# Performance work log

Hardware: AMD Instinct MI355X
Metric: run time of the kernel (lower is better)

Reference implementation:

```python
import jax, jax.numpy as jnp
import numpy as np

NUM_HEADS = 12
ALPHA = 0.5
TANH_CLIP = 5.0


def setup_inputs() -> dict:
    key = jax.random.key(0)
    k1, k2, k3, k4, k5 = jax.random.split(key, 5)
    B, N, C = 8, 1024, 768
    x = jax.random.normal(k1, (B, N, C), dtype=jnp.float32)
    # qkv: Linear(C -> 3C), proj: Linear(C -> C); torch stores weight as [out, in]
    s = 1.0 / np.sqrt(C)
    qkv_w = jax.random.normal(k2, (3 * C, C), dtype=jnp.float32) * s
    qkv_b = jax.random.normal(k3, (3 * C,), dtype=jnp.float32) * 0.02
    proj_w = jax.random.normal(k4, (C, C), dtype=jnp.float32) * s
    proj_b = jax.random.normal(k5, (C,), dtype=jnp.float32) * 0.02
    return {"x": x, "qkv_w": qkv_w, "qkv_b": qkv_b, "proj_w": proj_w, "proj_b": proj_b}


def reference(x, qkv_w, qkv_b, proj_w, proj_b):
    B, N, C = x.shape
    H = NUM_HEADS
    D = C // H
    scale = D ** -0.5
    # qkv projection -> [B, N, 3, H, D] -> q/k/v each [B, H, N, D]
    qkv = (x @ qkv_w.T + qkv_b).reshape(B, N, 3, H, D)
    qkv = jnp.transpose(qkv, (2, 0, 3, 1, 4))
    q, k, v = qkv[0], qkv[1], qkv[2]
    # pre-softmax scores [B, H, N, N]
    scores = jnp.einsum("bhnd,bhmd->bhnm", q * scale, k)
    scores_t = jnp.swapaxes(scores, -2, -1)
    scores_sym = 0.5 * (scores + scores_t)
    scores_asym = 0.5 * (scores - scores_t)
    scores = scores_sym + ALPHA * scores_asym
    # gamma_mode == 'approx'
    gamma = np.sqrt((1.0 + ALPHA ** 2) / 2.0)
    scores = scores / gamma
    # tanh clip
    scores = TANH_CLIP * jnp.tanh(scores / TANH_CLIP)
    attn = jax.nn.softmax(scores, axis=-1)
    out = jnp.einsum("bhnm,bhmd->bhnd", attn, v)  # [B, H, N, D]
    out = jnp.transpose(out, (0, 2, 1, 3)).reshape(B, N, C)
    return out @ proj_w.T + proj_b
```

## Files before the change

### kernel.cpp

```cpp
#include <hip/hip_runtime.h>
#include <hip/hip_bf16.h>
#include <stdint.h>

typedef unsigned short u16;
typedef __attribute__((ext_vector_type(8))) short bf16x8;
typedef __attribute__((ext_vector_type(4))) float f32x4;

#define LDS_AS(p) ((__attribute__((address_space(3))) void*)(p))
#define GLB_AS(p) ((__attribute__((address_space(1))) void*)(p))

__device__ __forceinline__ u16 f2bf(float f) {
  union { float f; uint32_t u; } v; v.f = f;
  uint32_t u = v.u;
  u += 0x7fffu + ((u >> 16) & 1u);
  return (u16)(u >> 16);
}

__device__ __forceinline__ float exp2_fast(float x) {
  float r;
  asm("v_exp_f32 %0, %1" : "=v"(r) : "v"(x));
  return r;
}

__device__ __forceinline__ float bits2f(uint32_t u) {
  union { uint32_t u; float f; } v; v.u = u; return v.f;
}
__device__ __forceinline__ uint32_t f2bits(float f) {
  union { float f; uint32_t u; } v; v.f = f; return v.u;
}
__device__ __forceinline__ uint32_t pack_hi16(uint32_t lo_src, uint32_t hi_src) {
  return __builtin_amdgcn_perm(hi_src, lo_src, 0x07060302u);
}

__device__ __forceinline__ void cvt8(const float* __restrict__ s, u16* __restrict__ d) {
  const float4* sv = (const float4*)s;
  float4 a = sv[0], b = sv[1];
  uint4 o;
  o.x = (uint32_t)f2bf(a.x) | ((uint32_t)f2bf(a.y) << 16);
  o.y = (uint32_t)f2bf(a.z) | ((uint32_t)f2bf(a.w) << 16);
  o.z = (uint32_t)f2bf(b.x) | ((uint32_t)f2bf(b.y) << 16);
  o.w = (uint32_t)f2bf(b.z) | ((uint32_t)f2bf(b.w) << 16);
  *(uint4*)d = o;
}

__global__ __launch_bounds__(256) void k_convert(
    const float* __restrict__ x, const float* __restrict__ wq, const float* __restrict__ wp,
    u16* __restrict__ xb, u16* __restrict__ wqb, u16* __restrict__ wpb) {
  int tid = blockIdx.x * 256 + threadIdx.x;
  int np  = gridDim.x * 256;
  for (int i = tid; i < (8192*768)/8; i += np) cvt8(x  + (size_t)i*8, xb  + (size_t)i*8);
  for (int i = tid; i < (2304*768)/8; i += np) cvt8(wq + (size_t)i*8, wqb + (size_t)i*8);
  for (int i = tid; i < (768*768)/8;  i += np) cvt8(wp + (size_t)i*8, wpb + (size_t)i*8);
}

template<bool SWAP>
__device__ __forceinline__ void gemm_core(const u16* __restrict__ A,
                                          const u16* __restrict__ B,
                                          u16* As, u16* Bs,
                                          int rowA0, int rowB0,
                                          f32x4 acc[4][4]) {
  const int t  = threadIdx.x;
  const int lane = t & 63;
  const int wv = t >> 6;
  const int wr = wv >> 1, wc = wv & 1;
  const int lr = lane & 15, lg = lane >> 4;

#define GSTAGE(KT, BUF)                                                                         \
  {                                                                                             \
    _Pragma("unroll")                                                                           \
    for (int p = 0; p < 2; ++p) {                                                               \
      int idx = p * 256 + t;                                                                    \
      int row = idx >> 2;                                                                       \
      int cc  = (idx & 3) ^ ((row >> 1) & 3);                                                   \
      __builtin_amdgcn_global_load_lds(GLB_AS(A + (size_t)(rowA0 + row) * 768 + (KT) * 32 + cc * 8), \
                                       LDS_AS(As + (BUF) * 4096 + idx * 8), 16, 0, 0);          \
    }                                                                                           \
    _Pragma("unroll")                                                                           \
    for (int p = 0; p < 2; ++p) {                                                               \
      int idx = p * 256 + t;                                                                    \
      int row = idx >> 2;                                                                       \
      int cc  = (idx & 3) ^ ((row >> 1) & 3);                                                   \
      __builtin_amdgcn_global_load_lds(GLB_AS(B + (size_t)(rowB0 + row) * 768 + (KT) * 32 + cc * 8), \
                                       LDS_AS(Bs + (BUF) * 4096 + idx * 8), 16, 0, 0);          \
    }                                                                                           \
  }

  GSTAGE(0, 0);

#pragma unroll 1
  for (int kt = 0; kt < 24; ++kt) {
    const int cur = kt & 1;
    __syncthreads();

    if (kt < 23) GSTAGE(kt + 1, cur ^ 1);

    const u16* Ab = As + cur * 4096;
    const u16* Bb = Bs + cur * 4096;
    bf16x8 af[4], bf_[4];
#pragma unroll
    for (int mi = 0; mi < 4; ++mi) {
      int row = wr * 64 + mi * 16 + lr;
      int cc  = lg ^ ((row >> 1) & 3);
      af[mi] = *(const bf16x8*)(Ab + row * 32 + cc * 8);
    }
#pragma unroll
    for (int ni = 0; ni < 4; ++ni) {
      int row = wc * 64 + ni * 16 + lr;
      int cc  = lg ^ ((row >> 1) & 3);
      bf_[ni] = *(const bf16x8*)(Bb + row * 32 + cc * 8);
    }
#pragma unroll
    for (int mi = 0; mi < 4; ++mi)
#pragma unroll
      for (int ni = 0; ni < 4; ++ni) {
        if (SWAP)
          acc[mi][ni] = __builtin_amdgcn_mfma_f32_16x16x32_bf16(bf_[ni], af[mi], acc[mi][ni], 0, 0, 0);
        else
          acc[mi][ni] = __builtin_amdgcn_mfma_f32_16x16x32_bf16(af[mi], bf_[ni], acc[mi][ni], 0, 0, 0);
      }
  }
#undef GSTAGE
}

__global__ __launch_bounds__(256) void k_gemm_qkv(
    const u16* __restrict__ Aq, const u16* __restrict__ Bw, const float* __restrict__ bias,
    u16* __restrict__ Qh, u16* __restrict__ Kh, u16* __restrict__ Vt) {
  __shared__ u16 As[2 * 128 * 32];
  __shared__ u16 Bs[2 * 128 * 32];
  int bid = blockIdx.x;
  int wg  = (bid & 7) * 144 + (bid >> 3);
  int bx  = wg % 18, by = wg / 18;

  const int t = threadIdx.x, lane = t & 63, wv = t >> 6;
  const int wr = wv >> 1, wc = wv & 1, lr = lane & 15, lg = lane >> 4;
  const int tsec = bx / 6;
  const int colBase = bx * 128 + wc * 64;

  const float gam = 0.7905694150420949f;
  const float rC1 = __builtin_sqrtf(0.57707801636f);
  const float sc1 = __builtin_sqrtf(0.09375f / gam) * rC1;
  const float sc2 = __builtin_sqrtf(0.03125f / gam) * rC1;

  f32x4 acc[4][4];
#pragma unroll
  for (int mi = 0; mi < 4; ++mi)
#pragma unroll
    for (int ni = 0; ni < 4; ++ni) acc[mi][ni] = (f32x4){0.f, 0.f, 0.f, 0.f};

  if (tsec < 2) {
    gemm_core<true>(Aq, Bw, As, Bs, by * 128, bx * 128, acc);

    float4 bv4[4];
#pragma unroll
    for (int ni = 0; ni < 4; ++ni)
      bv4[ni] = *(const float4*)(bias + colBase + ni * 16 + lg * 4);

#pragma unroll
    for (int mi = 0; mi < 4; ++mi) {
      int n = by * 128 + wr * 64 + mi * 16 + lr;
      int b = n >> 10, nn = n & 1023;
#pragma unroll
      for (int ni = 0; ni < 4; ++ni) {
        int fs = colBase - tsec * 768 + ni * 16 + lg * 4;
        int h = fs >> 6, d = fs & 63;
        size_t rowq = ((size_t)(b * 12 + h) * 1024 + nn) * 128;
        float v0 = acc[mi][ni][0] + bv4[ni].x;
        float v1 = acc[mi][ni][1] + bv4[ni].y;
        float v2 = acc[mi][ni][2] + bv4[ni].z;
        float v3 = acc[mi][ni][3] + bv4[ni].w;
        uint2 wq_, wk_;
        wq_.x = (uint32_t)f2bf(v0 * sc1) | ((uint32_t)f2bf(v1 * sc1) << 16);
        wq_.y = (uint32_t)f2bf(v2 * sc1) | ((uint32_t)f2bf(v3 * sc1) << 16);
        wk_.x = (uint32_t)f2bf(v0 * sc2) | ((uint32_t)f2bf(v1 * sc2) << 16);
        wk_.y = (uint32_t)f2bf(v2 * sc2) | ((uint32_t)f2bf(v3 * sc2) << 16);
        if (tsec == 0) {
          *(uint2*)(Qh + rowq + d)      = wq_;
          *(uint2*)(Kh + rowq + 64 + d) = wk_;
        } else {
          *(uint2*)(Kh + rowq + d)      = wq_;
          *(uint2*)(Qh + rowq + 64 + d) = wk_;
        }
      }
    }
  } else {
    gemm_core<false>(Aq, Bw, As, Bs, by * 128, bx * 128, acc);

    float bv[4];
#pragma unroll
    for (int ni = 0; ni < 4; ++ni) bv[ni] = bias[colBase + ni * 16 + lr];

#pragma unroll
    for (int mi = 0; mi < 4; ++mi) {
      int tok0 = by * 128 + wr * 64 + mi * 16 + lg * 4;
      int b = tok0 >> 10, n0 = tok0 & 1023;
#pragma unroll
      for (int ni = 0; ni < 4; ++ni) {
        int fs = colBase - 2 * 768 + ni * 16 + lr;
        int h = fs >> 6, d = fs & 63;
        float v0 = acc[mi][ni][0] + bv[ni];
        float v1 = acc[mi][ni][1] + bv[ni];
        float v2 = acc[mi][ni][2] + bv[ni];
        float v3 = acc[mi][ni][3] + bv[ni];
        uint2 w;
        w.x = (uint32_t)f2bf(v0) | ((uint32_t)f2bf(v1) << 16);
        w.y = (uint32_t)f2bf(v2) | ((uint32_t)f2bf(v3) << 16);
        *(uint2*)(Vt + ((size_t)((b * 12 + h) * 64 + d)) * 1024 + n0) = w;
      }
    }
  }
}

__global__ __launch_bounds__(256, 3) void k_attn(
    const u16* __restrict__ Qh, const u16* __restrict__ Kh, const u16* __restrict__ Vt,
    u16* __restrict__ attn) {
  __shared__ u16 Ks[64 * 128];
  __shared__ u16 Vs[2][64 * 64];
  __shared__ u16 Ps[4][2][32 * 40];

  int bid = blockIdx.x;
  int wg = (bid & 7) * 96 + (bid >> 3);
  int bh = wg >> 3, qb = wg & 7;
  int b = bh / 12, h = bh % 12;

  const int t = threadIdx.x, lane = t & 63, wv = t >> 6;
  const int lr = lane & 15, lg = lane >> 4;

  const size_t khb = (size_t)bh * 1024 * 128;
  const size_t vtb = (size_t)bh * 64 * 1024;

  bf16x8 qf[2][4];
  {
    const u16* qp = Qh + ((size_t)bh * 1024 + qb * 128 + wv * 32 + lr) * 128 + lg * 8;
#pragma unroll
    for (int it = 0; it < 2; ++it)
#pragma unroll
      for (int kk = 0; kk < 4; ++kk)
        qf[it][kk] = *(const bf16x8*)(qp + it * 16 * 128 + kk * 32);
  }

#define STAGE_K(KT)                                                                            \
  {                                                                                            \
    _Pragma("unroll")                                                                          \
    for (int p = 0; p < 4; ++p) {                                                              \
      int idx = p * 256 + t;                                                                   \
      int row = idx >> 4;                                                                      \
      int cc  = (idx & 15) ^ (row & 7);                                                        \
      __builtin_amdgcn_global_load_lds(GLB_AS(Kh + khb + (size_t)((KT) * 64 + row) * 128 + cc * 8), \
                                       LDS_AS(Ks + idx * 8), 16, 0, 0);                        \
    }                                                                                          \
  }
#define STAGE_V(KT, BUF)                                                                       \
  {                                                                                            \
    _Pragma("unroll")                                                                          \
    for (int p = 0; p < 2; ++p) {                                                              \
      int idx = p * 256 + t;                                                                   \
      int d   = idx >> 3;                                                                      \
      int g   = (idx & 7) ^ (d & 7);                                                           \
      __builtin_amdgcn_global_load_lds(GLB_AS(Vt + vtb + (size_t)d * 1024 + (KT) * 64 + g * 8),\
                                       LDS_AS(Vs[BUF] + idx * 8), 16, 0, 0);                   \
    }                                                                                          \
  }

  STAGE_V(0, 0);
  STAGE_K(0);

  f32x4 acc_o[4][2];
#pragma unroll
  for (int dt = 0; dt < 4; ++dt)
#pragma unroll
    for (int it = 0; it < 2; ++it) acc_o[dt][it] = (f32x4){0.f, 0.f, 0.f, 0.f};
  float dsum[2] = {0.f, 0.f};

  const float C2 = -14.4269504089f;

#pragma unroll 1
  for (int kt = 0; kt < 16; ++kt) {
    const int cur = kt & 1;
    __syncthreads();

    if (kt < 15) STAGE_V(kt + 1, cur ^ 1);

    f32x4 accs[4][2];
#pragma unroll
    for (int jt = 0; jt < 4; ++jt)
#pragma unroll
      for (int it = 0; it < 2; ++it) accs[jt][it] = (f32x4){0.f, 0.f, 0.f, 0.f};
    __builtin_amdgcn_s_setprio(1);
#pragma unroll
    for (int jt = 0; jt < 4; ++jt) {
#pragma unroll
      for (int kk = 0; kk < 4; ++kk) {
        int row = jt * 16 + lr;
        int cc  = (kk * 4 + lg) ^ (row & 7);
        bf16x8 kf = *(const bf16x8*)(Ks + row * 128 + cc * 8);
#pragma unroll
        for (int it = 0; it < 2; ++it)
          accs[jt][it] = __builtin_amdgcn_mfma_f32_16x16x32_bf16(kf, qf[it][kk], accs[jt][it], 0, 0, 0);
      }
    }
    __builtin_amdgcn_s_setprio(0);

    __syncthreads();
    if (kt < 15) STAGE_K(kt + 1);

#pragma unroll
    for (int jt = 0; jt < 4; ++jt) {
      const int ks = jt >> 1, jtl = jt & 1;
#pragma unroll
      for (int it = 0; it < 2; ++it) {
        float p0 = exp2_fast(C2 * __builtin_amdgcn_rcpf(exp2_fast(accs[jt][it][0]) + 1.0f));
        float p1 = exp2_fast(C2 * __builtin_amdgcn_rcpf(exp2_fast(accs[jt][it][1]) + 1.0f));
        float p2 = exp2_fast(C2 * __builtin_amdgcn_rcpf(exp2_fast(accs[jt][it][2]) + 1.0f));
        float p3 = exp2_fast(C2 * __builtin_amdgcn_rcpf(exp2_fast(accs[jt][it][3]) + 1.0f));
        uint32_t a0 = f2bits(p0), a1 = f2bits(p1), a2 = f2bits(p2), a3 = f2bits(p3);
        uint2 w;
        w.x = pack_hi16(a0, a1);
        w.y = pack_hi16(a2, a3);
        dsum[it] += (bits2f(a0 & 0xFFFF0000u) + bits2f(a1 & 0xFFFF0000u))
                  + (bits2f(a2 & 0xFFFF0000u) + bits2f(a3 & 0xFFFF0000u));
        *(uint2*)(&Ps[wv][ks][(it * 16 + lr) * 40 + jtl * 16 + lg * 4]) = w;
      }
    }

    asm volatile("" ::: "memory");

    {
      const u16* V0 = Vs[cur];
#pragma unroll
      for (int ks = 0; ks < 2; ++ks) {
        bf16x8 pa[2];
#pragma unroll
        for (int it = 0; it < 2; ++it)
          pa[it] = *(const bf16x8*)(&Ps[wv][ks][(it * 16 + lr) * 40 + lg * 8]);
        __builtin_amdgcn_s_setprio(1);
#pragma unroll
        for (int dt = 0; dt < 4; ++dt) {
          int row  = dt * 16 + lr;
          int slot = (ks * 4 + lg) ^ (lr & 7);
          bf16x8 vf = *(const bf16x8*)(V0 + row * 64 + slot * 8);
#pragma unroll
          for (int it = 0; it < 2; ++it)
            acc_o[dt][it] = __builtin_amdgcn_mfma_f32_16x16x32_bf16(vf, pa[it], acc_o[dt][it], 0, 0, 0);
        }
        __builtin_amdgcn_s_setprio(0);
      }
    }
  }
#undef STAGE_K
#undef STAGE_V

  float rinv[2];
#pragma unroll
  for (int it = 0; it < 2; ++it) {
    float v = dsum[it];
    v += __shfl_xor(v, 16);
    v += __shfl_xor(v, 32);
    rinv[it] = __builtin_amdgcn_rcpf(v);
  }

#pragma unroll
  for (int dt = 0; dt < 4; ++dt) {
#pragma unroll
    for (int it = 0; it < 2; ++it) {
      float v0 = acc_o[dt][it][0] * rinv[it];
      float v1 = acc_o[dt][it][1] * rinv[it];
      float v2 = acc_o[dt][it][2] * rinv[it];
      float v3 = acc_o[dt][it][3] * rinv[it];
      uint2 w;
      w.x = (uint32_t)f2bf(v0) | ((uint32_t)f2bf(v1) << 16);
      w.y = (uint32_t)f2bf(v2) | ((uint32_t)f2bf(v3) << 16);
      int n = qb * 128 + wv * 32 + it * 16 + lr;
      *(uint2*)(attn + ((size_t)(b * 1024 + n)) * 768 + h * 64 + dt * 16 + lg * 4) = w;
    }
  }
}

__global__ __launch_bounds__(256) void k_gemm_proj(
    const u16* __restrict__ Ain, const u16* __restrict__ Bw, const float* __restrict__ bias,
    float* __restrict__ out) {
  __shared__ u16 As[2 * 128 * 32];
  __shared__ u16 Bs[2 * 128 * 32];
  int bid = blockIdx.x;
  int wg  = (bid & 7) * 48 + (bid >> 3);
  int bx  = wg % 6, by = wg / 6;

  f32x4 acc[4][4];
#pragma unroll
  for (int mi = 0; mi < 4; ++mi)
#pragma unroll
    for (int ni = 0; ni < 4; ++ni) acc[mi][ni] = (f32x4){0.f, 0.f, 0.f, 0.f};

  gemm_core<false>(Ain, Bw, As, Bs, by * 128, bx * 128, acc);

  const int t = threadIdx.x, lane = t & 63, wv = t >> 6;
  const int wr = wv >> 1, wc = wv & 1, lr = lane & 15, lg = lane >> 4;
  const int col0 = bx * 128 + wc * 64;

  float bv[4];
#pragma unroll
  for (int ni = 0; ni < 4; ++ni) bv[ni] = bias[col0 + ni * 16 + lr];

#pragma unroll
  for (int mi = 0; mi < 4; ++mi) {
    int tok0 = by * 128 + wr * 64 + mi * 16 + lg * 4;
#pragma unroll
    for (int ni = 0; ni < 4; ++ni) {
      int col = col0 + ni * 16 + lr;
#pragma unroll
      for (int r = 0; r < 4; ++r) {
        out[(size_t)(tok0 + r) * 768 + col] = acc[mi][ni][r] + bv[ni];
      }
    }
  }
}

extern "C" void kernel_launch(void* const* d_in, const int* in_sizes, int n_in,
                              void* d_out, int out_size, void* d_ws, size_t ws_size,
                              hipStream_t stream) {
  (void)in_sizes; (void)n_in; (void)out_size;
  const float* x      = (const float*)d_in[0];
  const float* qkv_w  = (const float*)d_in[1];
  const float* qkv_b  = (const float*)d_in[2];
  const float* proj_w = (const float*)d_in[3];
  const float* proj_b = (const float*)d_in[4];
  float* out = (float*)d_out;

  uint8_t* ws = (uint8_t*)d_ws;
  u16* xb  = (u16*)(ws + 0);
  u16* wqb = (u16*)(ws + 12582912);
  u16* wpb = (u16*)(ws + 16121856);
  u16* Qh  = (u16*)(ws + 17301504);
  u16* Kh  = (u16*)(ws + 42467328);
  u16* Vt  = (u16*)(ws + 80216064);
  if (ws_size < 92798976) return;

  u16* attnb = xb;

  k_convert<<<1024, 256, 0, stream>>>(x, qkv_w, proj_w, xb, wqb, wpb);
  k_gemm_qkv<<<1152, 256, 0, stream>>>(xb, wqb, qkv_b, Qh, Kh, Vt);
  k_attn<<<768, 256, 0, stream>>>(Qh, Kh, Vt, attnb);
  k_gemm_proj<<<384, 256, 0, stream>>>(attnb, wpb, proj_b, out);
}
```

Measured before the change: 143.6 us.

## Interleave softmax halves with QK^T and PV MFMA halves in attention loop

Splits each KV tile's QK^T, softmax and PV work into two halves and orders them as QK0, SM0, QK1, sync, PV0, SM1, PV1. The aim is to let the transcendental-heavy softmax VALU work overlap with MFMA work from the other half, rather than running as a separate serial phase. Softmax of the first half now happens before the second barrier and K restage. This depends on the compiler and hardware actually co-issuing the two kinds of work, and may change register pressure.

```diff
diff --git a/kernel.cpp b/kernel.cpp
--- a/kernel.cpp
+++ b/kernel.cpp
@@ -261,6 +261,67 @@
     }                                                                                          \
   }
 
+#define SM_HALF(KS)                                                                            \
+  {                                                                                            \
+    _Pragma("unroll")                                                                          \
+    for (int jtl = 0; jtl < 2; ++jtl) {                                                        \
+      const int jt = (KS) * 2 + jtl;                                                           \
+      _Pragma("unroll")                                                                        \
+      for (int it = 0; it < 2; ++it) {                                                         \
+        float p0 = exp2_fast(C2 * __builtin_amdgcn_rcpf(exp2_fast(accs[jt][it][0]) + 1.0f));   \
+        float p1 = exp2_fast(C2 * __builtin_amdgcn_rcpf(exp2_fast(accs[jt][it][1]) + 1.0f));   \
+        float p2 = exp2_fast(C2 * __builtin_amdgcn_rcpf(exp2_fast(accs[jt][it][2]) + 1.0f));   \
+        float p3 = exp2_fast(C2 * __builtin_amdgcn_rcpf(exp2_fast(accs[jt][it][3]) + 1.0f));   \
+        uint32_t a0 = f2bits(p0), a1 = f2bits(p1), a2 = f2bits(p2), a3 = f2bits(p3);           \
+        uint2 w;                                                                               \
+        w.x = pack_hi16(a0, a1);                                                               \
+        w.y = pack_hi16(a2, a3);                                                               \
+        dsum[it] += (bits2f(a0 & 0xFFFF0000u) + bits2f(a1 & 0xFFFF0000u))                      \
+                  + (bits2f(a2 & 0xFFFF0000u) + bits2f(a3 & 0xFFFF0000u));                     \
+        *(uint2*)(&Ps[wv][KS][(it * 16 + lr) * 40 + jtl * 16 + lg * 4]) = w;                   \
+      }                                                                                        \
+    }                                                                                          \
+  }
+
+#define QKT_HALF(HALF)                                                                         \
+  {                                                                                            \
+    __builtin_amdgcn_s_setprio(1);                                                             \
+    _Pragma("unroll")                                                                          \
+    for (int jtl = 0; jtl < 2; ++jtl) {                                                        \
+      const int jt = (HALF) * 2 + jtl;                                                         \
+      _Pragma("unroll")                                                                        \
+      for (int kk = 0; kk < 4; ++kk) {                                                         \
+        int row = jt * 16 + lr;                                                                \
+        int cc  = (kk * 4 + lg) ^ (row & 7);                                                   \
+        bf16x8 kf = *(const bf16x8*)(Ks + row * 128 + cc * 8);                                 \
+        _Pragma("unroll")                                                                      \
+        for (int it = 0; it < 2; ++it)                                                         \
+          accs[jt][it] = __builtin_amdgcn_mfma_f32_16x16x32_bf16(kf, qf[it][kk], accs[jt][it], 0, 0, 0); \
+      }                                                                                        \
+    }                                                                                          \
+    __builtin_amdgcn_s_setprio(0);                                                             \
+  }
+
+#define PV_HALF(KS)                                                                            \
+  {                                                                                            \
+    const u16* V0 = Vs[cur];                                                                   \
+    bf16x8 pa[2];                                                                              \
+    _Pragma("unroll")                                                                          \
+    for (int it = 0; it < 2; ++it)                                                             \
+      pa[it] = *(const bf16x8*)(&Ps[wv][KS][(it * 16 + lr) * 40 + lg * 8]);                    \
+    __builtin_amdgcn_s_setprio(1);                                                             \
+    _Pragma("unroll")                                                                          \
+    for (int dt = 0; dt < 4; ++dt) {                                                           \
+      int row  = dt * 16 + lr;                                                                 \
+      int slot = ((KS) * 4 + lg) ^ (lr & 7);                                                   \
+      bf16x8 vf = *(const bf16x8*)(V0 + row * 64 + slot * 8);                                  \
+      _Pragma("unroll")                                                                        \
+      for (int it = 0; it < 2; ++it)                                                           \
+        acc_o[dt][it] = __builtin_amdgcn_mfma_f32_16x16x32_bf16(vf, pa[it], acc_o[dt][it], 0, 0, 0); \
+    }                                                                                          \
+    __builtin_amdgcn_s_setprio(0);                                                             \
+  }
+
   STAGE_V(0, 0);
   STAGE_K(0);
 
@@ -285,69 +346,28 @@
     for (int jt = 0; jt < 4; ++jt)
 #pragma unroll
       for (int it = 0; it < 2; ++it) accs[jt][it] = (f32x4){0.f, 0.f, 0.f, 0.f};
-    __builtin_amdgcn_s_setprio(1);
-#pragma unroll
-    for (int jt = 0; jt < 4; ++jt) {
-#pragma unroll
-      for (int kk = 0; kk < 4; ++kk) {
-        int row = jt * 16 + lr;
-        int cc  = (kk * 4 + lg) ^ (row & 7);
-        bf16x8 kf = *(const bf16x8*)(Ks + row * 128 + cc * 8);
-#pragma unroll
-        for (int it = 0; it < 2; ++it)
-          accs[jt][it] = __builtin_amdgcn_mfma_f32_16x16x32_bf16(kf, qf[it][kk], accs[jt][it], 0, 0, 0);
-      }
-    }
-    __builtin_amdgcn_s_setprio(0);
+
+    QKT_HALF(0);
+    SM_HALF(0);
+    QKT_HALF(1);
 
     __syncthreads();
     if (kt < 15) STAGE_K(kt + 1);
 
-#pragma unroll
-    for (int jt = 0; jt < 4; ++jt) {
-      const int ks = jt >> 1, jtl = jt & 1;
-#pragma unroll
-      for (int it = 0; it < 2; ++it) {
-        float p0 = exp2_fast(C2 * __builtin_amdgcn_rcpf(exp2_fast(accs[jt][it][0]) + 1.0f));
-        float p1 = exp2_fast(C2 * __builtin_amdgcn_rcpf(exp2_fast(accs[jt][it][1]) + 1.0f));
-        float p2 = exp2_fast(C2 * __builtin_amdgcn_rcpf(exp2_fast(accs[jt][it][2]) + 1.0f));
-        float p3 = exp2_fast(C2 * __builtin_amdgcn_rcpf(exp2_fast(accs[jt][it][3]) + 1.0f));
-        uint32_t a0 = f2bits(p0), a1 = f2bits(p1), a2 = f2bits(p2), a3 = f2bits(p3);
-        uint2 w;
-        w.x = pack_hi16(a0, a1);
-        w.y = pack_hi16(a2, a3);
-        dsum[it] += (bits2f(a0 & 0xFFFF0000u) + bits2f(a1 & 0xFFFF0000u))
-                  + (bits2f(a2 & 0xFFFF0000u) + bits2f(a3 & 0xFFFF0000u));
-        *(uint2*)(&Ps[wv][ks][(it * 16 + lr) * 40 + jtl * 16 + lg * 4]) = w;
-      }
-    }
-
     asm volatile("" ::: "memory");
 
-    {
-      const u16* V0 = Vs[cur];
-#pragma unroll
-      for (int ks = 0; ks < 2; ++ks) {
-        bf16x8 pa[2];
-#pragma unroll
-        for (int it = 0; it < 2; ++it)
-          pa[it] = *(const bf16x8*)(&Ps[wv][ks][(it * 16 + lr) * 40 + lg * 8]);
-        __builtin_amdgcn_s_setprio(1);
-#pragma unroll
-        for (int dt = 0; dt < 4; ++dt) {
-          int row  = dt * 16 + lr;
-          int slot = (ks * 4 + lg) ^ (lr & 7);
-          bf16x8 vf = *(const bf16x8*)(V0 + row * 64 + slot * 8);
-#pragma unroll
-          for (int it = 0; it < 2; ++it)
-            acc_o[dt][it] = __builtin_amdgcn_mfma_f32_16x16x32_bf16(vf, pa[it], acc_o[dt][it], 0, 0, 0);
-        }
-        __builtin_amdgcn_s_setprio(0);
-      }
-    }
+    PV_HALF(0);
+    SM_HALF(1);
+
+    asm volatile("" ::: "memory");
+
+    PV_HALF(1);
   }
 #undef STAGE_K
 #undef STAGE_V
+#undef SM_HALF
+#undef QKT_HALF
+#undef PV_HALF
 
   float rinv[2];
 #pragma unroll
```

New measurement: 145.0 us. About the same (+0.9%).
